# Kernel optimization log

Hardware: AMD Instinct MI355X
Metric: run time of the kernel (lower is better)

Reference implementation:

```python
import jax, jax.numpy as jnp
import numpy as np

N_NODES = 65536
N_EDGES = 1048576
IN_F = 128
HID_F = 128
OUT_F = 128


def setup_inputs() -> dict:
    key = jax.random.key(0)
    ks = jax.random.split(key, 8)
    feat = jax.random.normal(ks[0], (N_NODES, IN_F), dtype=jnp.float32)
    eweight = jax.random.uniform(ks[1], (N_EDGES, 1), dtype=jnp.float32)
    W1 = jax.random.normal(ks[2], (IN_F, HID_F), dtype=jnp.float32) * (1.0 / np.sqrt(IN_F))
    b1 = jnp.zeros((HID_F,), dtype=jnp.float32)
    W2 = jax.random.normal(ks[3], (HID_F, OUT_F), dtype=jnp.float32) * (1.0 / np.sqrt(HID_F))
    b2 = jnp.zeros((OUT_F,), dtype=jnp.float32)
    src = jax.random.randint(ks[4], (N_EDGES,), 0, N_NODES, dtype=jnp.int32)
    dst = jax.random.randint(ks[5], (N_EDGES,), 0, N_NODES, dtype=jnp.int32)
    return {"feat": feat, "eweight": eweight, "W1": W1, "b1": b1,
            "W2": W2, "b2": b2, "src": src, "dst": dst}


def _degrees(src, dst, n_nodes):
    ones = jnp.ones(src.shape[0], dtype=jnp.float32)
    deg_out = jax.ops.segment_sum(ones, src, num_segments=n_nodes)
    deg_in = jax.ops.segment_sum(ones, dst, num_segments=n_nodes)
    # DGL GraphConv clamps degree to min 1 before norm='both'
    return jnp.clip(deg_out, 1.0, None), jnp.clip(deg_in, 1.0, None)


def _graph_conv(feat, W, b, src, dst, out_norm, in_norm, n_nodes):
    # DGL GraphConv, norm='both': D_out^{-1/2} x -> x W -> spmm sum -> D_in^{-1/2} -> + b
    h = feat * out_norm[:, None]
    h = h @ W
    agg = jax.ops.segment_sum(h[src], dst, num_segments=n_nodes)
    return agg * in_norm[:, None] + b


def reference(feat, eweight, W1, b1, W2, b2, src, dst):
    n = feat.shape[0]
    deg_out, deg_in = _degrees(src, dst, n)
    out_norm = jax.lax.rsqrt(deg_out)
    in_norm = jax.lax.rsqrt(deg_in)
    h = _graph_conv(feat, W1, b1, src, dst, out_norm, in_norm, n)
    h = jax.nn.relu(h)
    h = _graph_conv(h, W2, b2, src, dst, out_norm, in_norm, n)
    # final update_all: u_mul_e + sum (eweight given)
    msg = h[src] * eweight  # [E, OUT_F]
    return jax.ops.segment_sum(msg, dst, num_segments=n)
```

## Files before the change

kernel.cpp:

```cpp
#include <hip/hip_runtime.h>

#define F 128
#define NBA 512
#define NBS 128
#define COARSE 256
#define CAP_BIN 4864
#define CAP_CSR 5632

typedef unsigned int uint;
typedef unsigned short ushort;
typedef unsigned char uchar;
typedef __attribute__((ext_vector_type(8))) short short8;
typedef __attribute__((ext_vector_type(8))) unsigned short ushort8;
typedef __attribute__((ext_vector_type(4))) float floatx4;

__device__ __forceinline__ ushort f2bf(float f) {
  uint u = __float_as_uint(f);
  u += 0x7fffu + ((u >> 16) & 1u);
  return (ushort)(u >> 16);
}

__global__ __launch_bounds__(256) void w_prep(const float* __restrict__ W1,
                                              const float* __restrict__ W2,
                                              ushort* __restrict__ W1t,
                                              ushort* __restrict__ W2t,
                                              int* __restrict__ cursorD,
                                              int* __restrict__ cursorS) {
  int b = blockIdx.x;
  if (b == 0) cursorD[threadIdx.x] = 0;
  if (b == 1) cursorS[threadIdx.x] = 0;
  const float* W = (b < 64) ? W1 : W2;
  ushort* Wt = (b < 64) ? W1t : W2t;
  int idx = (b & 63) * 256 + threadIdx.x;
  int k = idx >> 7, n = idx & 127;
  Wt[n * F + k] = f2bf(W[idx]);
}

__global__ __launch_bounds__(256) void bin_edges(
    const int* __restrict__ src, const int* __restrict__ dst,
    const float* __restrict__ ew, int E,
    int* __restrict__ cursorD, int* __restrict__ cursorS,
    uint2* __restrict__ slotD, uchar* __restrict__ srcF) {
  __shared__ int cnt[4][COARSE];
  __shared__ int base[COARSE];
  bool isD = blockIdx.x < NBA;
  int blk = isD ? blockIdx.x : blockIdx.x - NBA;
  int nblk = isD ? NBA : NBS;
  const int* key = isD ? dst : src;
  int* cursor = isD ? cursorD : cursorS;
  int wave = threadIdx.x >> 6;
  for (int i = threadIdx.x; i < 4 * COARSE; i += 256) ((int*)cnt)[i] = 0;
  __syncthreads();
  int chunk = (E + nblk - 1) / nblk;
  int s0 = blk * chunk, s1 = min(E, s0 + chunk);
  for (int i = s0 + threadIdx.x; i < s1; i += 256)
    atomicAdd(&cnt[wave][key[i] >> 8], 1);
  __syncthreads();
  if (threadIdx.x < COARSE) {
    int b = threadIdx.x;
    int tot = cnt[0][b] + cnt[1][b] + cnt[2][b] + cnt[3][b];
    base[b] = tot ? atomicAdd(&cursor[b], tot) : 0;
    cnt[0][b] = 0;
  }
  __syncthreads();
  if (isD) {
    for (int i = s0 + threadIdx.x; i < s1; i += 256) {
      int d = dst[i];
      int bin = d >> 8;
      int p = base[bin] + atomicAdd(&cnt[0][bin], 1);
      if (p < CAP_BIN) {
        uint2 v;
        v.x = (uint)(src[i] & 0xffff) | ((uint)f2bf(ew[i]) << 16);
        v.y = (uint)(d & 255);
        slotD[(size_t)bin * CAP_BIN + p] = v;
      }
    }
  } else {
    for (int i = s0 + threadIdx.x; i < s1; i += 256) {
      int s = src[i];
      int bin = s >> 8;
      int p = base[bin] + atomicAdd(&cnt[0][bin], 1);
      if (p < CAP_BIN) srcF[(size_t)bin * CAP_BIN + p] = (uchar)(s & 255);
    }
  }
}

__global__ __launch_bounds__(1024) void bucket_csr(
    const uint2* __restrict__ slotD, const int* __restrict__ cursorD,
    int2* __restrict__ rowRange, float* __restrict__ inNorm, uint* __restrict__ csr,
    const uchar* __restrict__ srcF, const int* __restrict__ cursorS,
    float* __restrict__ outNorm) {
  __shared__ int hist[256], base[256], cur[256];
  int t = threadIdx.x;
  if (blockIdx.x >= COARSE) {
    int b = blockIdx.x - COARSE;
    int lo = b * CAP_BIN;
    int cntS = min(cursorS[b], CAP_BIN);
    if (t < 256) hist[t] = 0;
    __syncthreads();
    for (int i = lo + t; i < lo + cntS; i += 1024)
      atomicAdd(&hist[srcF[i]], 1);
    __syncthreads();
    if (t < 256) outNorm[b * 256 + t] = rsqrtf((float)max(hist[t], 1));
    return;
  }
  int b = blockIdx.x;
  int lo = b * CAP_BIN;
  int cntD = min(cursorD[b], CAP_BIN);
  int hi = lo + cntD;
  if (t < 256) hist[t] = 0;
  __syncthreads();
  for (int i = lo + t; i < hi; i += 1024)
    atomicAdd(&hist[slotD[i].y], 1);
  __syncthreads();
  if (t < 256) base[t] = (hist[t] + 3) & ~3;
  __syncthreads();
  for (int off = 1; off < 256; off <<= 1) {
    int x = 0;
    if (t < 256 && t >= off) x = base[t - off];
    __syncthreads();
    if (t < 256) base[t] += x;
    __syncthreads();
  }
  if (t < 256) {
    int v = hist[t];
    int sz4 = (v + 3) & ~3;
    int st = b * CAP_CSR + base[t] - sz4;
    base[t] = st;
    cur[t] = 0;
    int node = b * 256 + t;
    rowRange[node] = make_int2(st, v);
    inNorm[node] = rsqrtf((float)max(v, 1));
    for (int p = st + v; p < st + sz4; ++p) csr[p] = 0x80000000u;
  }
  __syncthreads();
  for (int i = lo + t; i < hi; i += 1024) {
    uint2 v = slotD[i];
    int fine = v.y;
    int p = base[fine] + atomicAdd(&cur[fine], 1);
    csr[p] = v.x;
  }
}

template <bool BF16IN>
__global__ __launch_bounds__(256) void gemm_mfma(
    const void* __restrict__ Xv, const float* __restrict__ scale,
    const ushort* __restrict__ Wt, ushort* __restrict__ Y) {
  __shared__ ushort sA[128 * 136];
  __shared__ ushort sB[128 * 136];
  int t = threadIdx.x;
  int row0 = blockIdx.x * 128;

  {
    int r = t >> 1, hf = t & 1;
    ushort* ap = sA + r * 136 + hf * 64;
    if (BF16IN) {
      const ushort* xp = (const ushort*)Xv + (size_t)(row0 + r) * F + hf * 64;
#pragma unroll
      for (int j = 0; j < 8; ++j)
        *(ushort8*)(ap + j * 8) = *(const ushort8*)(xp + j * 8);
    } else {
      const float* xp = (const float*)Xv + (size_t)(row0 + r) * F + hf * 64;
      float s = scale[row0 + r];
#pragma unroll
      for (int j = 0; j < 8; ++j) {
        float4 v0 = *(const float4*)(xp + j * 8);
        float4 v1 = *(const float4*)(xp + j * 8 + 4);
        ushort8 o;
        o[0] = f2bf(v0.x * s); o[1] = f2bf(v0.y * s); o[2] = f2bf(v0.z * s); o[3] = f2bf(v0.w * s);
        o[4] = f2bf(v1.x * s); o[5] = f2bf(v1.y * s); o[6] = f2bf(v1.z * s); o[7] = f2bf(v1.w * s);
        *(ushort8*)(ap + j * 8) = o;
      }
    }
  }
  {
    int n = t >> 1, hf = t & 1;
    const ushort* wp = Wt + n * F + hf * 64;
    ushort* bp = sB + n * 136 + hf * 64;
#pragma unroll
    for (int j = 0; j < 8; ++j)
      *(ushort8*)(bp + j * 8) = *(const ushort8*)(wp + j * 8);
  }
  __syncthreads();

  int lane = t & 63, wave = t >> 6;
  int quad = lane >> 4, l16 = lane & 15;
  int mrow0 = wave * 32;

  floatx4 acc[2][8];
#pragma unroll
  for (int a = 0; a < 2; ++a)
#pragma unroll
    for (int c = 0; c < 8; ++c) acc[a][c] = (floatx4){0.f, 0.f, 0.f, 0.f};

#pragma unroll
  for (int kc = 0; kc < 128; kc += 32) {
    short8 afrag[2], bfrag[8];
#pragma unroll
    for (int a = 0; a < 2; ++a)
      afrag[a] = *(const short8*)(sA + (mrow0 + a * 16 + l16) * 136 + kc + quad * 8);
#pragma unroll
    for (int c = 0; c < 8; ++c)
      bfrag[c] = *(const short8*)(sB + (c * 16 + l16) * 136 + kc + quad * 8);
#pragma unroll
    for (int a = 0; a < 2; ++a)
#pragma unroll
      for (int c = 0; c < 8; ++c)
        acc[a][c] = __builtin_amdgcn_mfma_f32_16x16x32_bf16(afrag[a], bfrag[c], acc[a][c], 0, 0, 0);
  }

#pragma unroll
  for (int a = 0; a < 2; ++a)
#pragma unroll
    for (int c = 0; c < 8; ++c)
#pragma unroll
      for (int r = 0; r < 4; ++r) {
        int row = row0 + mrow0 + a * 16 + quad * 4 + r;
        int col = c * 16 + l16;
        Y[(size_t)row * F + col] = f2bf(acc[a][c][r]);
      }
}


template <bool EW, bool NB, bool RELU, bool PS, bool OUT_BF16>
__global__ __launch_bounds__(256) void spmm(
    const ushort* __restrict__ hb, const int2* __restrict__ rowRange,
    const uint* __restrict__ csr, const float* __restrict__ inNorm,
    const float* __restrict__ bias, const float* __restrict__ postScale,
    void* __restrict__ outv) {
  int lane = threadIdx.x & 63;
  int g = lane >> 4;
  int j = lane & 15;
  int n = blockIdx.x * 16 + (threadIdx.x >> 6) * 4 + g;
  int2 r = rowRange[n];
  int len4 = (r.y + 3) & ~3;
  const char* hbB = (const char*)hb;
  uint joff = (uint)j << 4;
  float acc[8] = {0.f, 0.f, 0.f, 0.f, 0.f, 0.f, 0.f, 0.f};

#define GQ(e, c, q)                                                      \
  {                                                                      \
    uint ei = (e);                                                       \
    c = *(const uint4*)(hbB + (((ei & 0xffffu) << 8) | joff));           \
    q = EW ? __uint_as_float(ei & 0xffff0000u)                           \
           : ((int)ei >= 0 ? 1.0f : 0.0f);                               \
  }
#define ACC8(c, q)                                                      \
  {                                                                     \
    acc[0] = fmaf(__uint_as_float(c.x << 16), q, acc[0]);               \
    acc[1] = fmaf(__uint_as_float(c.x & 0xffff0000u), q, acc[1]);       \
    acc[2] = fmaf(__uint_as_float(c.y << 16), q, acc[2]);               \
    acc[3] = fmaf(__uint_as_float(c.y & 0xffff0000u), q, acc[3]);       \
    acc[4] = fmaf(__uint_as_float(c.z << 16), q, acc[4]);               \
    acc[5] = fmaf(__uint_as_float(c.z & 0xffff0000u), q, acc[5]);       \
    acc[6] = fmaf(__uint_as_float(c.w << 16), q, acc[6]);               \
    acc[7] = fmaf(__uint_as_float(c.w & 0xffff0000u), q, acc[7]);       \
  }

  int i = 0;
  while (i + 8 <= len4) {
    uint4 e0 = *(const uint4*)(csr + r.x + i);
    uint4 e1 = *(const uint4*)(csr + r.x + i + 4);
    uint4 c0, c1, c2, c3, c4, c5, c6, c7;
    float q0, q1, q2, q3, q4, q5, q6, q7;
    GQ(e0.x, c0, q0) GQ(e0.y, c1, q1) GQ(e0.z, c2, q2) GQ(e0.w, c3, q3)
    GQ(e1.x, c4, q4) GQ(e1.y, c5, q5) GQ(e1.z, c6, q6) GQ(e1.w, c7, q7)
    ACC8(c0, q0) ACC8(c1, q1) ACC8(c2, q2) ACC8(c3, q3)
    ACC8(c4, q4) ACC8(c5, q5) ACC8(c6, q6) ACC8(c7, q7)
    i += 8;
  }
  if (i < len4) {
    uint4 e0 = *(const uint4*)(csr + r.x + i);
    uint4 c0, c1, c2, c3;
    float q0, q1, q2, q3;
    GQ(e0.x, c0, q0) GQ(e0.y, c1, q1) GQ(e0.z, c2, q2) GQ(e0.w, c3, q3)
    ACC8(c0, q0) ACC8(c1, q1) ACC8(c2, q2) ACC8(c3, q3)
  }
#undef GQ
#undef ACC8

  if (NB) {
    float sc = inNorm[n];
    float4 b0 = ((const float4*)bias)[2 * j];
    float4 b1 = ((const float4*)bias)[2 * j + 1];
    float bb[8] = {b0.x, b0.y, b0.z, b0.w, b1.x, b1.y, b1.z, b1.w};
#pragma unroll
    for (int k = 0; k < 8; ++k) {
      acc[k] = fmaf(acc[k], sc, bb[k]);
      if (RELU) acc[k] = fmaxf(acc[k], 0.f);
    }
    if (PS) {
      float o = postScale[n];
#pragma unroll
      for (int k = 0; k < 8; ++k) acc[k] *= o;
    }
  }
  if (OUT_BF16) {
    uint4 o;
    o.x = ((uint)f2bf(acc[1]) << 16) | (uint)f2bf(acc[0]);
    o.y = ((uint)f2bf(acc[3]) << 16) | (uint)f2bf(acc[2]);
    o.z = ((uint)f2bf(acc[5]) << 16) | (uint)f2bf(acc[4]);
    o.w = ((uint)f2bf(acc[7]) << 16) | (uint)f2bf(acc[6]);
    ((uint4*)outv)[(size_t)n * 16 + j] = o;
  } else {
    float4 lo = {acc[0], acc[1], acc[2], acc[3]};
    float4 hi = {acc[4], acc[5], acc[6], acc[7]};
    ((float4*)outv)[(size_t)n * 32 + 2 * j] = lo;
    ((float4*)outv)[(size_t)n * 32 + 2 * j + 1] = hi;
  }
}


extern "C" void kernel_launch(void* const* d_in, const int* in_sizes, int n_in,
                              void* d_out, int out_size, void* d_ws, size_t ws_size,
                              hipStream_t stream) {
  const float* feat = (const float*)d_in[0];
  const float* ew   = (const float*)d_in[1];
  const float* W1   = (const float*)d_in[2];
  const float* b1   = (const float*)d_in[3];
  const float* W2   = (const float*)d_in[4];
  const float* b2   = (const float*)d_in[5];
  const int*   src  = (const int*)d_in[6];
  const int*   dst  = (const int*)d_in[7];
  const int N = in_sizes[0] / F;
  const int E = in_sizes[6];
  float* out = (float*)d_out;

  char* ws = (char*)d_ws;
  size_t off = 0;
  auto alloc = [&](size_t bytes) {
    void* p = ws + off;
    off += (bytes + 255) & ~(size_t)255;
    return p;
  };
  int2*   rowRange = (int2*)alloc((size_t)N * 8);
  float*  inNorm   = (float*)alloc((size_t)N * 4);
  float*  outNorm  = (float*)alloc((size_t)N * 4);
  ushort* W1t      = (ushort*)alloc((size_t)F * F * 2);
  ushort* W2t      = (ushort*)alloc((size_t)F * F * 2);
  int*    cursorD  = (int*)alloc(COARSE * 4);
  int*    cursorS  = (int*)alloc(COARSE * 4);
  uint*   csr      = (uint*)alloc((size_t)COARSE * CAP_CSR * 4);
  ushort* bufAb    = (ushort*)alloc((size_t)N * F * 2);
  ushort* bufBb    = (ushort*)alloc((size_t)N * F * 2);
  ushort* bufCb    = (ushort*)alloc((size_t)N * F * 2);
  if (off > ws_size) return;

  uint2* slotD;
  uchar* srcF;
  {
    char* tp = (char*)bufBb;
    size_t toff = 0;
    auto talloc = [&](size_t bytes) {
      void* p = tp + toff;
      toff += (bytes + 255) & ~(size_t)255;
      return p;
    };
    slotD = (uint2*)talloc((size_t)COARSE * CAP_BIN * 8);
    srcF  = (uchar*)talloc((size_t)COARSE * CAP_BIN);
  }

  w_prep<<<128, 256, 0, stream>>>(W1, W2, W1t, W2t, cursorD, cursorS);
  bin_edges<<<NBA + NBS, 256, 0, stream>>>(src, dst, ew, E, cursorD, cursorS, slotD, srcF);
  bucket_csr<<<2 * COARSE, 1024, 0, stream>>>(slotD, cursorD, rowRange, inNorm, csr,
                                              srcF, cursorS, outNorm);

  gemm_mfma<false><<<N / 128, 256, 0, stream>>>(feat, outNorm, W1t, bufAb);
  spmm<false, true, true, true, true><<<N / 16, 256, 0, stream>>>(
      bufAb, rowRange, csr, inNorm, b1, outNorm, bufBb);
  gemm_mfma<true><<<N / 128, 256, 0, stream>>>(bufBb, nullptr, W2t, bufAb);
  spmm<false, true, false, false, true><<<N / 16, 256, 0, stream>>>(
      bufAb, rowRange, csr, inNorm, b2, nullptr, bufCb);
  spmm<true, false, false, false, false><<<N / 16, 256, 0, stream>>>(
      bufCb, rowRange, csr, nullptr, nullptr, nullptr, out);
}
```

Measured before the change: 269.3 us.

## Split bf16 feature matrices into 32-column planes for cache-local SpMM gathers

New measurement: 264.8 us. No clear change (-1.7%).

```diff
diff --git a/kernel.cpp b/kernel.cpp
--- a/kernel.cpp
+++ b/kernel.cpp
@@ -1,6 +1,7 @@
 #include <hip/hip_runtime.h>
 
 #define F 128
+#define NN 65536
 #define NBA 512
 #define NBS 128
 #define COARSE 256
@@ -19,6 +20,7 @@
   u += 0x7fffu + ((u >> 16) & 1u);
   return (ushort)(u >> 16);
 }
+
 
 __global__ __launch_bounds__(256) void w_prep(const float* __restrict__ W1,
                                               const float* __restrict__ W2,
@@ -155,10 +157,13 @@
     int r = t >> 1, hf = t & 1;
     ushort* ap = sA + r * 136 + hf * 64;
     if (BF16IN) {
-      const ushort* xp = (const ushort*)Xv + (size_t)(row0 + r) * F + hf * 64;
-#pragma unroll
-      for (int j = 0; j < 8; ++j)
-        *(ushort8*)(ap + j * 8) = *(const ushort8*)(xp + j * 8);
+      const ushort* xp = (const ushort*)Xv;
+#pragma unroll
+      for (int j = 0; j < 8; ++j) {
+        int q = 2 * hf + (j >> 2);
+        *(ushort8*)(ap + j * 8) =
+            *(const ushort8*)(xp + ((size_t)q * NN + row0 + r) * 32 + (j & 3) * 8);
+      }
     } else {
       const float* xp = (const float*)Xv + (size_t)(row0 + r) * F + hf * 64;
       float s = scale[row0 + r];
@@ -217,7 +222,7 @@
       for (int r = 0; r < 4; ++r) {
         int row = row0 + mrow0 + a * 16 + quad * 4 + r;
         int col = c * 16 + l16;
-        Y[(size_t)row * F + col] = f2bf(acc[a][c][r]);
+        Y[((size_t)(col >> 5) * NN + row) * 32 + (col & 31)] = f2bf(acc[a][c][r]);
       }
 }
 
@@ -228,20 +233,23 @@
     const uint* __restrict__ csr, const float* __restrict__ inNorm,
     const float* __restrict__ bias, const float* __restrict__ postScale,
     void* __restrict__ outv) {
+  int bid = blockIdx.x;
+  int plane = (bid & 7) >> 1;
+  int chunk = ((bid >> 3) << 1) | (bid & 1);
   int lane = threadIdx.x & 63;
-  int g = lane >> 4;
-  int j = lane & 15;
-  int n = blockIdx.x * 16 + (threadIdx.x >> 6) * 4 + g;
+  int g = lane >> 2;
+  int j = lane & 3;
+  int n = chunk * 64 + (threadIdx.x >> 6) * 16 + g;
   int2 r = rowRange[n];
   int len4 = (r.y + 3) & ~3;
-  const char* hbB = (const char*)hb;
+  const char* pb = (const char*)hb + (size_t)plane * ((size_t)NN * 64);
   uint joff = (uint)j << 4;
   float acc[8] = {0.f, 0.f, 0.f, 0.f, 0.f, 0.f, 0.f, 0.f};
 
 #define GQ(e, c, q)                                                      \
   {                                                                      \
     uint ei = (e);                                                       \
-    c = *(const uint4*)(hbB + (((ei & 0xffffu) << 8) | joff));           \
+    c = *(const uint4*)(pb + (((ei & 0xffffu) << 6) | joff));            \
     q = EW ? __uint_as_float(ei & 0xffff0000u)                           \
            : ((int)ei >= 0 ? 1.0f : 0.0f);                               \
   }
@@ -281,8 +289,8 @@
 
   if (NB) {
     float sc = inNorm[n];
-    float4 b0 = ((const float4*)bias)[2 * j];
-    float4 b1 = ((const float4*)bias)[2 * j + 1];
+    float4 b0 = ((const float4*)bias)[plane * 8 + j * 2];
+    float4 b1 = ((const float4*)bias)[plane * 8 + j * 2 + 1];
     float bb[8] = {b0.x, b0.y, b0.z, b0.w, b1.x, b1.y, b1.z, b1.w};
 #pragma unroll
     for (int k = 0; k < 8; ++k) {
@@ -301,12 +309,12 @@
     o.y = ((uint)f2bf(acc[3]) << 16) | (uint)f2bf(acc[2]);
     o.z = ((uint)f2bf(acc[5]) << 16) | (uint)f2bf(acc[4]);
     o.w = ((uint)f2bf(acc[7]) << 16) | (uint)f2bf(acc[6]);
-    ((uint4*)outv)[(size_t)n * 16 + j] = o;
+    ((uint4*)outv)[((size_t)plane * NN + n) * 4 + j] = o;
   } else {
     float4 lo = {acc[0], acc[1], acc[2], acc[3]};
     float4 hi = {acc[4], acc[5], acc[6], acc[7]};
-    ((float4*)outv)[(size_t)n * 32 + 2 * j] = lo;
-    ((float4*)outv)[(size_t)n * 32 + 2 * j + 1] = hi;
+    ((float4*)outv)[(size_t)n * 32 + plane * 8 + j * 2] = lo;
+    ((float4*)outv)[(size_t)n * 32 + plane * 8 + j * 2 + 1] = hi;
   }
 }
 
```
